# Optimization experiments

Hardware: AMD Instinct MI355X
Metric: run time of the kernel (lower is better)

Reference implementation:

```python
import jax, jax.numpy as jnp
import numpy as np

HEADS = 16
DIM_HEAD = 64
SCALE = DIM_HEAD ** -0.5


def setup_inputs() -> dict:
    key = jax.random.key(0)
    ks = jax.random.split(key, 5)
    b, n, dim = 2, 2048, 1024
    inner = HEADS * DIM_HEAD  # 1024
    std = dim ** -0.5
    return {
        "x": jax.random.normal(ks[0], (b, n, dim), jnp.float32),
        "ln_gamma": jnp.ones((dim,), jnp.float32),
        "ln_beta": jnp.zeros((dim,), jnp.float32),
        "W_qk": jax.random.normal(ks[1], (dim, 2 * inner), jnp.float32) * std,
        "W_v": jax.random.normal(ks[2], (dim, inner), jnp.float32) * std,
        "W_out": jax.random.normal(ks[3], (inner, dim), jnp.float32) * std,
        "b_out": jnp.zeros((dim,), jnp.float32),
    }


def _layernorm(x, gamma, beta, eps=1e-5):
    mu = jnp.mean(x, axis=-1, keepdims=True)
    var = jnp.var(x, axis=-1, keepdims=True)
    return (x - mu) * jax.lax.rsqrt(var + eps) * gamma + beta


def reference(x, ln_gamma, ln_beta, W_qk, W_v, W_out, b_out):
    b, n, dim = x.shape
    h, d = HEADS, DIM_HEAD
    xn = _layernorm(x, ln_gamma, ln_beta)
    qk = xn @ W_qk                      # [b, n, 2*h*d]
    q, k = jnp.split(qk, 2, axis=-1)    # each [b, n, h*d]
    v = xn @ W_v                        # [b, n, h*d]
    # b n (h d) -> b h n d
    q = q.reshape(b, n, h, d).transpose(0, 2, 1, 3)
    k = k.reshape(b, n, h, d).transpose(0, 2, 1, 3)
    v = v.reshape(b, n, h, d).transpose(0, 2, 1, 3)
    dots = jnp.einsum('bhid,bhjd->bhij', q, k) * SCALE
    attn = jax.nn.softmax(dots, axis=-1)
    out = jnp.einsum('bhij,bhjd->bhid', attn, v)
    out = out.transpose(0, 2, 1, 3).reshape(b, n, h * d)
    return out @ W_out + b_out
```

## Files before the change

### kernel.cpp

```cpp
#include <hip/hip_runtime.h>

#define HEADS 16
#define DHEAD 64
#define BATCH 2
#define SEQ   2048
#define DIM   1024
#define ROWS  (BATCH*SEQ)
#define SCALE_LOG2E 0.180336880f

typedef short v8s __attribute__((ext_vector_type(8)));
typedef float v4f __attribute__((ext_vector_type(4)));

__device__ __forceinline__ float fast_exp2(float x) {
    return __builtin_amdgcn_exp2f(x);
}

__device__ __forceinline__ unsigned short f2bf(float f) {
    unsigned u = __float_as_uint(f);
    u += 0x7FFFu + ((u >> 16) & 1u);
    return (unsigned short)(u >> 16);
}

__device__ __forceinline__ unsigned pk_bf2(float hi, float lo) {
    return __builtin_amdgcn_perm(__float_as_uint(hi), __float_as_uint(lo), 0x07060302u);
}

#define GLDS16(g, l) __builtin_amdgcn_global_load_lds( \
    (__attribute__((address_space(1))) void*)(g), \
    (__attribute__((address_space(3))) void*)(l), 16, 0, 0)

__global__ __launch_bounds__(256) void ln_kernel(const float* __restrict__ x,
                                                 const float* __restrict__ gamma,
                                                 const float* __restrict__ beta,
                                                 unsigned short* __restrict__ xn) {
    int row = blockIdx.x;
    const float* xr = x + (size_t)row * DIM;
    int t = threadIdx.x;
    float4 v = *(const float4*)(xr + t * 4);
    float s  = v.x + v.y + v.z + v.w;
    float sq = v.x * v.x + v.y * v.y + v.z * v.z + v.w * v.w;
#pragma unroll
    for (int off = 32; off > 0; off >>= 1) {
        s  += __shfl_down(s,  off, 64);
        sq += __shfl_down(sq, off, 64);
    }
    __shared__ float ss[4], ssq[4];
    int wave = t >> 6, lane = t & 63;
    if (lane == 0) { ss[wave] = s; ssq[wave] = sq; }
    __syncthreads();
    float tot  = ss[0] + ss[1] + ss[2] + ss[3];
    float totq = ssq[0] + ssq[1] + ssq[2] + ssq[3];
    float mean = tot * (1.f / DIM);
    float var  = totq * (1.f / DIM) - mean * mean;
    float rstd = rsqrtf(var + 1e-5f);
    float4 g = *(const float4*)(gamma + t * 4);
    float4 bb = *(const float4*)(beta + t * 4);
    ushort4 o;
    o.x = f2bf((v.x - mean) * rstd * g.x + bb.x);
    o.y = f2bf((v.y - mean) * rstd * g.y + bb.y);
    o.z = f2bf((v.z - mean) * rstd * g.z + bb.z);
    o.w = f2bf((v.w - mean) * rstd * g.w + bb.w);
    *(ushort4*)(xn + (size_t)row * DIM + t * 4) = o;
}

__global__ __launch_bounds__(256) void tr_all_kernel(const float* __restrict__ Wqk,
                                                     const float* __restrict__ Wv,
                                                     const float* __restrict__ Wout,
                                                     unsigned short* __restrict__ Tqk,
                                                     unsigned short* __restrict__ Tv,
                                                     unsigned short* __restrict__ To) {
    int z = blockIdx.z;
    const float* W = (z == 0) ? Wqk : (z == 1) ? Wv : Wout;
    unsigned short* Wt = (z == 0) ? Tqk : (z == 1) ? Tv : To;
    int Nw = (z == 0) ? 2048 : 1024;
    int n0 = blockIdx.x * 64, k0 = blockIdx.y * 64;
    if (n0 >= Nw) return;
    __shared__ float tile[64][65];
    int tid = threadIdx.x;
#pragma unroll
    for (int l = 0; l < 4; ++l) {
        int kk = (tid >> 4) + l * 16;
        int nn = (tid & 15) * 4;
        float4 v = *(const float4*)(W + (size_t)(k0 + kk) * Nw + n0 + nn);
        tile[kk][nn + 0] = v.x; tile[kk][nn + 1] = v.y;
        tile[kk][nn + 2] = v.z; tile[kk][nn + 3] = v.w;
    }
    __syncthreads();
#pragma unroll
    for (int l = 0; l < 4; ++l) {
        int cid = tid + l * 256;
        int nn = cid >> 4, kc = (cid & 15) * 4;
        ushort4 o;
        o.x = f2bf(tile[kc + 0][nn]);
        o.y = f2bf(tile[kc + 1][nn]);
        o.z = f2bf(tile[kc + 2][nn]);
        o.w = f2bf(tile[kc + 3][nn]);
        *(ushort4*)(Wt + (size_t)(n0 + nn) * DIM + k0 + kc) = o;
    }
}

template<int BN, bool SWAP>
__device__ __forceinline__ void mm_core2(const unsigned short* __restrict__ A,
                                         const unsigned short* __restrict__ Bt,
                                         int K, int aTile, int bTile,
                                         unsigned short (*As)[32],
                                         unsigned short (*Bs)[32],
                                         v4f (*acc)[4]) {
    constexpr int MI = (BN == 128) ? 4 : 2;
    int t = threadIdx.x;
    int w = t >> 6, L = t & 63, l15 = L & 15, quad = L >> 4;
    int aOff = (BN == 128) ? (w >> 1) * 64 : w * 32;
    int bOff = (BN == 128) ? (w & 1) * 64 : 0;
    int srow = L >> 2, schunk = (L & 3) * 8;
    for (int k0 = 0; k0 < K; k0 += 32) {
        __syncthreads();
#pragma unroll
        for (int j = 0; j < 2; ++j) {
            int g = w * 2 + j;
            GLDS16(A + (size_t)(aTile + g * 16 + srow) * K + k0 + schunk,
                   &As[g * 16][0]);
        }
#pragma unroll
        for (int j = 0; j < BN / 64; ++j) {
            int g = (BN == 128) ? (w * 2 + j) : w;
            GLDS16(Bt + (size_t)(bTile + g * 16 + srow) * K + k0 + schunk,
                   &Bs[g * 16][0]);
        }
        __syncthreads();
        v8s a[MI], b[4];
#pragma unroll
        for (int i = 0; i < MI; ++i) a[i] = *(const v8s*)&As[aOff + i * 16 + l15][quad * 8];
#pragma unroll
        for (int j = 0; j < 4; ++j) b[j] = *(const v8s*)&Bs[bOff + j * 16 + l15][quad * 8];
#pragma unroll
        for (int i = 0; i < MI; ++i)
#pragma unroll
            for (int j = 0; j < 4; ++j)
                acc[i][j] = SWAP
                    ? __builtin_amdgcn_mfma_f32_16x16x32_bf16(b[j], a[i], acc[i][j], 0, 0, 0)
                    : __builtin_amdgcn_mfma_f32_16x16x32_bf16(a[i], b[j], acc[i][j], 0, 0, 0);
    }
}

__global__ __launch_bounds__(256) void gemm_qkv_kernel(const unsigned short* __restrict__ A,
                                                       const unsigned short* __restrict__ Bt,
                                                       unsigned short* __restrict__ q_h,
                                                       unsigned short* __restrict__ k_h,
                                                       unsigned short* __restrict__ v_t) {
    __shared__ __align__(16) unsigned short As[128][32];
    __shared__ __align__(16) unsigned short Bs[128][32];
    int t = threadIdx.x, w = t >> 6, L = t & 63, l15 = L & 15, quad = L >> 4;
    int aTile = blockIdx.y * 128, bTile = blockIdx.x * 128;
    int aOff = (w >> 1) * 64, bOff = (w & 1) * 64;
    v4f acc[4][4] = {};
    if (bTile < 2048) {
        mm_core2<128, true>(A, Bt, DIM, aTile, bTile, As, Bs, acc);
#pragma unroll
        for (int j = 0; j < 4; ++j) {
            int col = bTile + bOff + j * 16 + quad * 4;
            unsigned short* dst = (col < 1024) ? q_h : k_h;
            int c = col & 1023;
            int h = c >> 6, d = c & 63;
#pragma unroll
            for (int i = 0; i < 4; ++i) {
                int m = aTile + aOff + i * 16 + l15;
                int b = m >> 11, seq = m & 2047;
                ushort4 o;
                o.x = f2bf(acc[i][j][0]); o.y = f2bf(acc[i][j][1]);
                o.z = f2bf(acc[i][j][2]); o.w = f2bf(acc[i][j][3]);
                *(ushort4*)(dst + (((size_t)(b * 16 + h)) * SEQ + seq) * 64 + d) = o;
            }
        }
    } else {
        mm_core2<128, false>(A, Bt, DIM, aTile, bTile, As, Bs, acc);
#pragma unroll
        for (int j = 0; j < 4; ++j) {
            int c = bTile + bOff + j * 16 + l15 - 2048;
            int h = c >> 6, d = c & 63;
#pragma unroll
            for (int i = 0; i < 4; ++i) {
                int m0 = aTile + aOff + i * 16 + quad * 4;
                int b = m0 >> 11, seq0 = m0 & 2047;
                ushort4 o;
                o.x = f2bf(acc[i][j][0]); o.y = f2bf(acc[i][j][1]);
                o.z = f2bf(acc[i][j][2]); o.w = f2bf(acc[i][j][3]);
                *(ushort4*)(v_t + (((size_t)(b * 16 + h)) * 64 + d) * SEQ + seq0) = o;
            }
        }
    }
}

__global__ __launch_bounds__(256) void gemm_out_kernel(const unsigned short* __restrict__ A,
                                                       const unsigned short* __restrict__ Bt,
                                                       const float* __restrict__ bias,
                                                       float* __restrict__ C) {
    __shared__ __align__(16) unsigned short As[128][32];
    __shared__ __align__(16) unsigned short Bs[64][32];
    int t = threadIdx.x, w = t >> 6, L = t & 63, l15 = L & 15, quad = L >> 4;
    int aTile = blockIdx.y * 128, bTile = blockIdx.x * 64;
    v4f acc[2][4] = {};
    mm_core2<64, true>(A, Bt, DIM, aTile, bTile, As, Bs, acc);
#pragma unroll
    for (int j = 0; j < 4; ++j) {
        int n = bTile + j * 16 + quad * 4;
        float4 bv = *(const float4*)(bias + n);
#pragma unroll
        for (int i = 0; i < 2; ++i) {
            int m = aTile + w * 32 + i * 16 + l15;
            float4 o = make_float4(acc[i][j][0] + bv.x, acc[i][j][1] + bv.y,
                                   acc[i][j][2] + bv.z, acc[i][j][3] + bv.w);
            *(float4*)(C + (size_t)m * DIM + n) = o;
        }
    }
}

__global__ __launch_bounds__(256) void attn_kernel(const unsigned short* __restrict__ q_h,
                                                   const unsigned short* __restrict__ k_h,
                                                   const unsigned short* __restrict__ v_t,
                                                   unsigned short* __restrict__ ao) {
    __shared__ __align__(16) unsigned short KF[8 * 64 * 8];
    __shared__ __align__(16) unsigned short VF[8 * 64 * 8];
    __shared__ __align__(16) unsigned short Pld[4][2][16 * 72];
    int qt = blockIdx.x, h = blockIdx.y, b = blockIdx.z;
    int bh = b * HEADS + h;
    int w = threadIdx.x >> 6;
    int L = threadIdx.x & 63, l15 = L & 15, quad = L >> 4;

    const unsigned short* qp = q_h + ((size_t)bh * SEQ + qt * 128 + w * 32 + l15) * 64 + quad * 8;
    v8s qf[2][2];
    qf[0][0] = *(const v8s*)(qp);
    qf[0][1] = *(const v8s*)(qp + 32);
    qf[1][0] = *(const v8s*)(qp + 16 * 64);
    qf[1][1] = *(const v8s*)(qp + 16 * 64 + 32);

    const unsigned short* kstage = k_h + ((size_t)bh * SEQ + w * 16 + l15) * 64 + quad * 8;
    const unsigned short* vstage = v_t + ((size_t)bh * 64 + w * 16 + l15) * SEQ + quad * 8;

    v4f o[2][4] = {};
    v4f lacc[2] = {};
    const short ob = (short)0x3F80;
    const v8s ones = {ob, ob, ob, ob, ob, ob, ob, ob};

    v8s ks0 = *(const v8s*)(kstage);
    v8s ks1 = *(const v8s*)(kstage + 32);
    v8s vs0 = *(const v8s*)(vstage);
    v8s vs1 = *(const v8s*)(vstage + 32);

    for (int j0 = 0; j0 < SEQ; j0 += 64) {
        __syncthreads();
        *(v8s*)&KF[((w * 2 + 0) * 64 + L) * 8] = ks0;
        *(v8s*)&KF[((w * 2 + 1) * 64 + L) * 8] = ks1;
        *(v8s*)&VF[((w * 2 + 0) * 64 + L) * 8] = vs0;
        *(v8s*)&VF[((w * 2 + 1) * 64 + L) * 8] = vs1;
        __syncthreads();
        if (j0 + 64 < SEQ) {
            ks0 = *(const v8s*)(kstage + (size_t)(j0 + 64) * 64);
            ks1 = *(const v8s*)(kstage + (size_t)(j0 + 64) * 64 + 32);
            vs0 = *(const v8s*)(vstage + j0 + 64);
            vs1 = *(const v8s*)(vstage + j0 + 64 + 32);
        }
        v8s kf[4][2], vf[4][2];
#pragma unroll
        for (int jt = 0; jt < 4; ++jt) {
            kf[jt][0] = *(const v8s*)&KF[((jt * 2 + 0) * 64 + L) * 8];
            kf[jt][1] = *(const v8s*)&KF[((jt * 2 + 1) * 64 + L) * 8];
            vf[jt][0] = *(const v8s*)&VF[((jt * 2 + 0) * 64 + L) * 8];
            vf[jt][1] = *(const v8s*)&VF[((jt * 2 + 1) * 64 + L) * 8];
        }
        v4f s[2][4] = {};
#pragma unroll
        for (int m = 0; m < 2; ++m)
#pragma unroll
            for (int jt = 0; jt < 4; ++jt) {
                s[m][jt] = __builtin_amdgcn_mfma_f32_16x16x32_bf16(kf[jt][0], qf[m][0], s[m][jt], 0, 0, 0);
                s[m][jt] = __builtin_amdgcn_mfma_f32_16x16x32_bf16(kf[jt][1], qf[m][1], s[m][jt], 0, 0, 0);
            }
#pragma unroll
        for (int m = 0; m < 2; ++m)
#pragma unroll
            for (int jt = 0; jt < 4; ++jt) {
                float p0 = fast_exp2(s[m][jt][0] * SCALE_LOG2E);
                float p1 = fast_exp2(s[m][jt][1] * SCALE_LOG2E);
                float p2 = fast_exp2(s[m][jt][2] * SCALE_LOG2E);
                float p3 = fast_exp2(s[m][jt][3] * SCALE_LOG2E);
                uint2 pk;
                pk.x = pk_bf2(p1, p0);
                pk.y = pk_bf2(p3, p2);
                *(uint2*)&Pld[w][m][l15 * 72 + jt * 16 + quad * 4] = pk;
            }
#pragma unroll
        for (int m = 0; m < 2; ++m) {
            v8s pb0 = *(const v8s*)&Pld[w][m][l15 * 72 + quad * 8];
            v8s pb1 = *(const v8s*)&Pld[w][m][l15 * 72 + 32 + quad * 8];
#pragma unroll
            for (int dt = 0; dt < 4; ++dt) {
                o[m][dt] = __builtin_amdgcn_mfma_f32_16x16x32_bf16(vf[dt][0], pb0, o[m][dt], 0, 0, 0);
                o[m][dt] = __builtin_amdgcn_mfma_f32_16x16x32_bf16(vf[dt][1], pb1, o[m][dt], 0, 0, 0);
            }
            lacc[m] = __builtin_amdgcn_mfma_f32_16x16x32_bf16(ones, pb0, lacc[m], 0, 0, 0);
            lacc[m] = __builtin_amdgcn_mfma_f32_16x16x32_bf16(ones, pb1, lacc[m], 0, 0, 0);
        }
    }
#pragma unroll
    for (int m = 0; m < 2; ++m) {
        float inv = 1.f / lacc[m][0];
        int rowg = b * SEQ + qt * 128 + w * 32 + m * 16 + l15;
#pragma unroll
        for (int dt = 0; dt < 4; ++dt) {
            ushort4 ov;
            ov.x = f2bf(o[m][dt][0] * inv);
            ov.y = f2bf(o[m][dt][1] * inv);
            ov.z = f2bf(o[m][dt][2] * inv);
            ov.w = f2bf(o[m][dt][3] * inv);
            *(ushort4*)(ao + (size_t)rowg * DIM + h * 64 + dt * 16 + quad * 4) = ov;
        }
    }
}

extern "C" void kernel_launch(void* const* d_in, const int* in_sizes, int n_in,
                              void* d_out, int out_size, void* d_ws, size_t ws_size,
                              hipStream_t stream) {
    const float* x     = (const float*)d_in[0];
    const float* gamma = (const float*)d_in[1];
    const float* beta  = (const float*)d_in[2];
    const float* Wqk   = (const float*)d_in[3];
    const float* Wv    = (const float*)d_in[4];
    const float* Wout  = (const float*)d_in[5];
    const float* bout  = (const float*)d_in[6];
    float* out = (float*)d_out;

    unsigned short* ws = (unsigned short*)d_ws;
    unsigned short* xn    = ws;
    unsigned short* Wt_qk = xn + (size_t)ROWS * DIM;
    unsigned short* Wt_v  = Wt_qk + (size_t)2048 * DIM;
    unsigned short* Wt_o  = Wt_v + (size_t)DIM * DIM;
    unsigned short* q_h   = Wt_o + (size_t)DIM * DIM;
    unsigned short* k_h   = q_h + (size_t)ROWS * DIM;
    unsigned short* v_t   = k_h + (size_t)ROWS * DIM;
    unsigned short* ao    = v_t + (size_t)ROWS * DIM;

    ln_kernel<<<ROWS, 256, 0, stream>>>(x, gamma, beta, xn);
    tr_all_kernel<<<dim3(32, 16, 3), 256, 0, stream>>>(Wqk, Wv, Wout, Wt_qk, Wt_v, Wt_o);
    gemm_qkv_kernel<<<dim3(3072 / 128, ROWS / 128), 256, 0, stream>>>(xn, Wt_qk, q_h, k_h, v_t);
    attn_kernel<<<dim3(SEQ / 128, HEADS, BATCH), 256, 0, stream>>>(q_h, k_h, v_t, ao);
    gemm_out_kernel<<<dim3(DIM / 64, ROWS / 128), 256, 0, stream>>>(ao, Wt_o, bout, out);
}
```

Measured before the change: 196.6 us.

## Double-buffer attention K/V via direct global-to-LDS loads, fold scale into Q

The attention kernel now keeps two LDS buffers for K and V and fills them with direct global-to-LDS loads (GLDS16) one tile ahead. This removes the register staging and the second barrier per iteration. The softmax scale times log2e is folded into Q in the QKV GEMM epilogue, which drops a multiply per score. The change also raises wave priority around the MFMA blocks and remaps block IDs so that consecutive blocks spread across XCDs by head and batch for better L2 locality. Rounding Q to bf16 after scaling changes numerics slightly. The loop has one barrier per iteration and relies on GLDS16 completing before the next barrier, which could race if waitcnt is not handled.

```diff
diff --git a/kernel.cpp b/kernel.cpp
--- a/kernel.cpp
+++ b/kernel.cpp
@@ -155,6 +155,7 @@
     v4f acc[4][4] = {};
     if (bTile < 2048) {
         mm_core2<128, true>(A, Bt, DIM, aTile, bTile, As, Bs, acc);
+        float sc = (bTile < 1024) ? SCALE_LOG2E : 1.0f;
 #pragma unroll
         for (int j = 0; j < 4; ++j) {
             int col = bTile + bOff + j * 16 + quad * 4;
@@ -166,8 +167,8 @@
                 int m = aTile + aOff + i * 16 + l15;
                 int b = m >> 11, seq = m & 2047;
                 ushort4 o;
-                o.x = f2bf(acc[i][j][0]); o.y = f2bf(acc[i][j][1]);
-                o.z = f2bf(acc[i][j][2]); o.w = f2bf(acc[i][j][3]);
+                o.x = f2bf(acc[i][j][0] * sc); o.y = f2bf(acc[i][j][1] * sc);
+                o.z = f2bf(acc[i][j][2] * sc); o.w = f2bf(acc[i][j][3] * sc);
                 *(ushort4*)(dst + (((size_t)(b * 16 + h)) * SEQ + seq) * 64 + d) = o;
             }
         }
@@ -218,10 +219,12 @@
                                                    const unsigned short* __restrict__ k_h,
                                                    const unsigned short* __restrict__ v_t,
                                                    unsigned short* __restrict__ ao) {
-    __shared__ __align__(16) unsigned short KF[8 * 64 * 8];
-    __shared__ __align__(16) unsigned short VF[8 * 64 * 8];
+    __shared__ __align__(16) unsigned short KF[2][8 * 64 * 8];
+    __shared__ __align__(16) unsigned short VF[2][8 * 64 * 8];
     __shared__ __align__(16) unsigned short Pld[4][2][16 * 72];
-    int qt = blockIdx.x, h = blockIdx.y, b = blockIdx.z;
+    int bid = blockIdx.x;
+    int wg = (bid & 7) * 64 + (bid >> 3);
+    int qt = wg & 15, h = (wg >> 4) & 15, b = wg >> 8;
     int bh = b * HEADS + h;
     int w = threadIdx.x >> 6;
     int L = threadIdx.x & 63, l15 = L & 15, quad = L >> 4;
@@ -233,41 +236,40 @@
     qf[1][0] = *(const v8s*)(qp + 16 * 64);
     qf[1][1] = *(const v8s*)(qp + 16 * 64 + 32);
 
-    const unsigned short* kstage = k_h + ((size_t)bh * SEQ + w * 16 + l15) * 64 + quad * 8;
-    const unsigned short* vstage = v_t + ((size_t)bh * 64 + w * 16 + l15) * SEQ + quad * 8;
+    const unsigned short* ksrc = k_h + ((size_t)bh * SEQ + w * 16 + l15) * 64 + quad * 8;
+    const unsigned short* vsrc = v_t + ((size_t)bh * 64 + w * 16 + l15) * SEQ + quad * 8;
+
+    GLDS16(ksrc,      &KF[0][(w * 2 + 0) * 512]);
+    GLDS16(ksrc + 32, &KF[0][(w * 2 + 1) * 512]);
+    GLDS16(vsrc,      &VF[0][(w * 2 + 0) * 512]);
+    GLDS16(vsrc + 32, &VF[0][(w * 2 + 1) * 512]);
 
     v4f o[2][4] = {};
     v4f lacc[2] = {};
     const short ob = (short)0x3F80;
     const v8s ones = {ob, ob, ob, ob, ob, ob, ob, ob};
 
-    v8s ks0 = *(const v8s*)(kstage);
-    v8s ks1 = *(const v8s*)(kstage + 32);
-    v8s vs0 = *(const v8s*)(vstage);
-    v8s vs1 = *(const v8s*)(vstage + 32);
-
+    int cur = 0;
     for (int j0 = 0; j0 < SEQ; j0 += 64) {
         __syncthreads();
-        *(v8s*)&KF[((w * 2 + 0) * 64 + L) * 8] = ks0;
-        *(v8s*)&KF[((w * 2 + 1) * 64 + L) * 8] = ks1;
-        *(v8s*)&VF[((w * 2 + 0) * 64 + L) * 8] = vs0;
-        *(v8s*)&VF[((w * 2 + 1) * 64 + L) * 8] = vs1;
-        __syncthreads();
         if (j0 + 64 < SEQ) {
-            ks0 = *(const v8s*)(kstage + (size_t)(j0 + 64) * 64);
-            ks1 = *(const v8s*)(kstage + (size_t)(j0 + 64) * 64 + 32);
-            vs0 = *(const v8s*)(vstage + j0 + 64);
-            vs1 = *(const v8s*)(vstage + j0 + 64 + 32);
+            const unsigned short* kn = ksrc + (size_t)(j0 + 64) * 64;
+            const unsigned short* vn = vsrc + (j0 + 64);
+            GLDS16(kn,      &KF[cur ^ 1][(w * 2 + 0) * 512]);
+            GLDS16(kn + 32, &KF[cur ^ 1][(w * 2 + 1) * 512]);
+            GLDS16(vn,      &VF[cur ^ 1][(w * 2 + 0) * 512]);
+            GLDS16(vn + 32, &VF[cur ^ 1][(w * 2 + 1) * 512]);
         }
         v8s kf[4][2], vf[4][2];
 #pragma unroll
         for (int jt = 0; jt < 4; ++jt) {
-            kf[jt][0] = *(const v8s*)&KF[((jt * 2 + 0) * 64 + L) * 8];
-            kf[jt][1] = *(const v8s*)&KF[((jt * 2 + 1) * 64 + L) * 8];
-            vf[jt][0] = *(const v8s*)&VF[((jt * 2 + 0) * 64 + L) * 8];
-            vf[jt][1] = *(const v8s*)&VF[((jt * 2 + 1) * 64 + L) * 8];
+            kf[jt][0] = *(const v8s*)&KF[cur][((jt * 2 + 0) * 64 + L) * 8];
+            kf[jt][1] = *(const v8s*)&KF[cur][((jt * 2 + 1) * 64 + L) * 8];
+            vf[jt][0] = *(const v8s*)&VF[cur][((jt * 2 + 0) * 64 + L) * 8];
+            vf[jt][1] = *(const v8s*)&VF[cur][((jt * 2 + 1) * 64 + L) * 8];
         }
         v4f s[2][4] = {};
+        __builtin_amdgcn_s_setprio(1);
 #pragma unroll
         for (int m = 0; m < 2; ++m)
 #pragma unroll
@@ -275,14 +277,15 @@
                 s[m][jt] = __builtin_amdgcn_mfma_f32_16x16x32_bf16(kf[jt][0], qf[m][0], s[m][jt], 0, 0, 0);
                 s[m][jt] = __builtin_amdgcn_mfma_f32_16x16x32_bf16(kf[jt][1], qf[m][1], s[m][jt], 0, 0, 0);
             }
+        __builtin_amdgcn_s_setprio(0);
 #pragma unroll
         for (int m = 0; m < 2; ++m)
 #pragma unroll
             for (int jt = 0; jt < 4; ++jt) {
-                float p0 = fast_exp2(s[m][jt][0] * SCALE_LOG2E);
-                float p1 = fast_exp2(s[m][jt][1] * SCALE_LOG2E);
-                float p2 = fast_exp2(s[m][jt][2] * SCALE_LOG2E);
-                float p3 = fast_exp2(s[m][jt][3] * SCALE_LOG2E);
+                float p0 = fast_exp2(s[m][jt][0]);
+                float p1 = fast_exp2(s[m][jt][1]);
+                float p2 = fast_exp2(s[m][jt][2]);
+                float p3 = fast_exp2(s[m][jt][3]);
                 uint2 pk;
                 pk.x = pk_bf2(p1, p0);
                 pk.y = pk_bf2(p3, p2);
@@ -292,6 +295,7 @@
         for (int m = 0; m < 2; ++m) {
             v8s pb0 = *(const v8s*)&Pld[w][m][l15 * 72 + quad * 8];
             v8s pb1 = *(const v8s*)&Pld[w][m][l15 * 72 + 32 + quad * 8];
+            __builtin_amdgcn_s_setprio(1);
 #pragma unroll
             for (int dt = 0; dt < 4; ++dt) {
                 o[m][dt] = __builtin_amdgcn_mfma_f32_16x16x32_bf16(vf[dt][0], pb0, o[m][dt], 0, 0, 0);
@@ -299,7 +303,9 @@
             }
             lacc[m] = __builtin_amdgcn_mfma_f32_16x16x32_bf16(ones, pb0, lacc[m], 0, 0, 0);
             lacc[m] = __builtin_amdgcn_mfma_f32_16x16x32_bf16(ones, pb1, lacc[m], 0, 0, 0);
-        }
+            __builtin_amdgcn_s_setprio(0);
+        }
+        cur ^= 1;
     }
 #pragma unroll
     for (int m = 0; m < 2; ++m) {
@@ -342,6 +348,6 @@
     ln_kernel<<<ROWS, 256, 0, stream>>>(x, gamma, beta, xn);
     tr_all_kernel<<<dim3(32, 16, 3), 256, 0, stream>>>(Wqk, Wv, Wout, Wt_qk, Wt_v, Wt_o);
     gemm_qkv_kernel<<<dim3(3072 / 128, ROWS / 128), 256, 0, stream>>>(xn, Wt_qk, q_h, k_h, v_t);
-    attn_kernel<<<dim3(SEQ / 128, HEADS, BATCH), 256, 0, stream>>>(q_h, k_h, v_t, ao);
+    attn_kernel<<<dim3(SEQ / 128 * HEADS * BATCH), 256, 0, stream>>>(q_h, k_h, v_t, ao);
     gemm_out_kernel<<<dim3(DIM / 64, ROWS / 128), 256, 0, stream>>>(ao, Wt_o, bout, out);
 }
```

After: 197.4 us. Within noise of the previous version (+0.4%).
